# Kernel tuning notes

Hardware: AMD Instinct MI355X
Metric: run time of the kernel (lower is better)

## Reference

```python
import jax, jax.numpy as jnp
import numpy as np

N = 30000          # mesh vertices
B = 5 * 16         # p_bins * t_bins geodesic patch bins
NEURONS = [16, 64, 64, 32]


def setup_inputs() -> dict:
    key = jax.random.key(0)
    ks = jax.random.split(key, 7)
    x = jax.random.normal(ks[0], (N, NEURONS[0]), dtype=jnp.float32)
    conn = jax.random.randint(ks[1], (N, B), 0, N)  # per-vertex per-bin source index
    s1 = 1.0 / np.sqrt(NEURONS[0])
    W1 = jax.random.uniform(ks[2], (NEURONS[0], NEURONS[1]), minval=-s1, maxval=s1, dtype=jnp.float32)
    s2 = 1.0 / np.sqrt(B * NEURONS[1])
    Wg1 = jax.random.uniform(ks[3], (B, NEURONS[1], NEURONS[2]), minval=-s2, maxval=s2, dtype=jnp.float32)
    b1 = jax.random.uniform(ks[4], (NEURONS[2],), minval=-s2, maxval=s2, dtype=jnp.float32)
    s3 = 1.0 / np.sqrt(B * NEURONS[2])
    Wg2 = jax.random.uniform(ks[5], (B, NEURONS[2], NEURONS[3]), minval=-s3, maxval=s3, dtype=jnp.float32)
    b2 = jax.random.uniform(ks[6], (NEURONS[3],), minval=-s3, maxval=s3, dtype=jnp.float32)
    return {"x": x, "W1": W1, "Wg1": Wg1, "b1": b1, "Wg2": Wg2, "b2": b2, "conn": conn}


def _geodesic(h, conn, Wg, b):
    # gather geodesic patch: [N, B, C_in], then per-bin contraction
    patches = h[conn]                               # irregular gather
    return jnp.einsum("nbi,bio->no", patches, Wg) + b


def reference(x, W1, Wg1, b1, Wg2, b2, conn):
    h = jax.nn.relu(x @ W1)                         # linear_1 (no bias, l_bias=False)
    h = jax.nn.relu(_geodesic(h, conn, Wg1, b1))    # GC_1 + relu
    res = _geodesic(h, conn, Wg2, b2)               # GC_2
    norm = jnp.linalg.norm(res, axis=-1, keepdims=True)
    return res / norm
```

## Files before the change

### kernel.cpp

```cpp
#include <hip/hip_runtime.h>
#include <stdint.h>
#include <stddef.h>


typedef __attribute__((ext_vector_type(8))) short bf16x8;
typedef __attribute__((ext_vector_type(4))) float f32x4;

#define BINS 80

static __device__ __forceinline__ unsigned short f2bf(float f) {
  union { float f; unsigned int u; } c; c.f = f;
  unsigned int u = c.u;
  return (unsigned short)((u + 0x7FFFu + ((u >> 16) & 1u)) >> 16);
}

__global__ __launch_bounds__(256) void k_lin1(const float* __restrict__ x,
                                              const float* __restrict__ W1,
                                              unsigned short* __restrict__ h1b, int n) {
  __shared__ float w1s[16 * 64];
  int tid = threadIdx.x;
  for (int i = tid; i < 16 * 64; i += 256) w1s[i] = W1[i];
  __syncthreads();
  int v = blockIdx.x * 256 + tid;
  if (v >= n) return;
  const float4* xp = (const float4*)(x + (size_t)v * 16);
  float4 x0 = xp[0], x1 = xp[1], x2 = xp[2], x3 = xp[3];
  float xr[16] = {x0.x, x0.y, x0.z, x0.w, x1.x, x1.y, x1.z, x1.w,
                  x2.x, x2.y, x2.z, x2.w, x3.x, x3.y, x3.z, x3.w};
  float acc[64];
#pragma unroll
  for (int o = 0; o < 64; ++o) acc[o] = 0.f;
#pragma unroll
  for (int i = 0; i < 16; ++i) {
    float xi = xr[i];
#pragma unroll
    for (int o = 0; o < 64; ++o) acc[o] = fmaf(xi, w1s[i * 64 + o], acc[o]);
  }
  unsigned short* hr = h1b + (size_t)v * 64;
#pragma unroll
  for (int o8 = 0; o8 < 8; ++o8) {
    bf16x8 pack;
#pragma unroll
    for (int j = 0; j < 8; ++j) pack[j] = (short)f2bf(fmaxf(acc[o8 * 8 + j], 0.f));
    *(bf16x8*)(hr + o8 * 8) = pack;
  }
}

__global__ __launch_bounds__(256) void k_wimg(const float* __restrict__ Wg,
                                              unsigned char* __restrict__ img,
                                              int O, int total) {
  int t = blockIdx.x * 256 + threadIdx.x;
  if (t >= total) return;
  int c = t & 7;
  int o = (t >> 3) % O;
  int b = t / (O * 8);
  int boff = (o * 128 + c * 16) ^ ((o & 7) << 4);
  bf16x8 pack;
#pragma unroll
  for (int j = 0; j < 8; ++j)
    pack[j] = (short)f2bf(Wg[(size_t)(b * 64 + c * 8 + j) * O + o]);
  *(bf16x8*)(img + (size_t)b * (O * 128) + boff) = pack;
}

template <int OT, bool DO_NORM>
__global__ __launch_bounds__(256) void k_geo(const unsigned short* __restrict__ hin,
                                             const unsigned char* __restrict__ wimg,
                                             const float* __restrict__ bias,
                                             const int* __restrict__ conn,
                                             void* __restrict__ outp, int n) {
  constexpr int TILEB = OT * 16 * 128;
  __shared__ int conn_s[64 * 81];
  __shared__ alignas(16) unsigned char wg_s[2][TILEB];

  const int tid = threadIdx.x;
  const int lane = tid & 63;
  const int wave = tid >> 6;
  const int ln15 = lane & 15;
  const int lq = lane >> 4;
  const int v0 = blockIdx.x * 64;

  for (int idx = tid; idx < 64 * BINS; idx += 256) {
    int v = idx / BINS;
    int c = idx - v * BINS;
    int vv = v0 + v;
    if (vv > n - 1) vv = n - 1;
    conn_s[v * 81 + c] = conn[(size_t)vv * BINS + c];
  }

  auto stage = [&](int bin, int buf) {
    const unsigned char* src = wimg + (size_t)bin * TILEB + wave * (TILEB / 4) + lane * 16;
    unsigned char* dst = &wg_s[buf][wave * (TILEB / 4)];
#pragma unroll
    for (int i = 0; i < TILEB / 4096; ++i) {
      __builtin_amdgcn_global_load_lds(
          (const __attribute__((address_space(1))) unsigned int*)(const void*)(src + i * 1024),
          (__attribute__((address_space(3))) unsigned int*)(void*)(dst + i * 1024),
          16, 0, 0);
    }
  };

  int boffs[OT][2];
#pragma unroll
  for (int ot = 0; ot < OT; ++ot)
#pragma unroll
    for (int s = 0; s < 2; ++s) {
      int o = ot * 16 + ln15;
      boffs[ot][s] = (o * 128 + s * 64 + lq * 16) ^ ((o & 7) << 4);
    }

  f32x4 acc[OT];
#pragma unroll
  for (int ot = 0; ot < OT; ++ot) acc[ot] = (f32x4){0.f, 0.f, 0.f, 0.f};

  stage(0, 0);
  __syncthreads();

  const int crow = (wave * 16 + ln15) * 81;
  const int koff = lq * 8;

  for (int b = 0; b < BINS; ++b) {
    int cur = b & 1;
    if (b + 1 < BINS) stage(b + 1, cur ^ 1);

    int cidx = conn_s[crow + b];
    const unsigned short* arow = hin + (size_t)cidx * 64 + koff;
    bf16x8 a0 = *(const bf16x8*)(arow);
    bf16x8 a1 = *(const bf16x8*)(arow + 32);

    const unsigned char* wb = wg_s[cur];
#pragma unroll
    for (int ot = 0; ot < OT; ++ot) {
      bf16x8 b0 = *(const bf16x8*)(wb + boffs[ot][0]);
      bf16x8 b1 = *(const bf16x8*)(wb + boffs[ot][1]);
      acc[ot] = __builtin_amdgcn_mfma_f32_16x16x32_bf16(a0, b0, acc[ot], 0, 0, 0);
      acc[ot] = __builtin_amdgcn_mfma_f32_16x16x32_bf16(a1, b1, acc[ot], 0, 0, 0);
    }
    __syncthreads();
  }

  if constexpr (!DO_NORM) {
    unsigned short* hout = (unsigned short*)outp;
#pragma unroll
    for (int ot = 0; ot < OT; ++ot) {
      float bo = bias[ot * 16 + ln15];
#pragma unroll
      for (int r = 0; r < 4; ++r) {
        int v = v0 + wave * 16 + lq * 4 + r;
        if (v < n) {
          float val = fmaxf(acc[ot][r] + bo, 0.f);
          hout[(size_t)v * 64 + ot * 16 + ln15] = f2bf(val);
        }
      }
    }
  } else {
    float* outf = (float*)outp;
    float bo0 = bias[ln15];
    float bo1 = bias[16 + ln15];
#pragma unroll
    for (int r = 0; r < 4; ++r) {
      float a = acc[0][r] + bo0;
      float c2 = acc[1][r] + bo1;
      float ss = a * a + c2 * c2;
      ss += __shfl_xor(ss, 1);
      ss += __shfl_xor(ss, 2);
      ss += __shfl_xor(ss, 4);
      ss += __shfl_xor(ss, 8);
      float inv = 1.0f / sqrtf(ss);
      int v = v0 + wave * 16 + lq * 4 + r;
      if (v < n) {
        outf[(size_t)v * 32 + ln15] = a * inv;
        outf[(size_t)v * 32 + 16 + ln15] = c2 * inv;
      }
    }
  }
}

extern "C" void kernel_launch(void* const* d_in, const int* in_sizes, int n_in,
                              void* d_out, int out_size, void* d_ws, size_t ws_size,
                              hipStream_t stream) {
  const float* x   = (const float*)d_in[0];
  const float* W1  = (const float*)d_in[1];
  const float* Wg1 = (const float*)d_in[2];
  const float* b1  = (const float*)d_in[3];
  const float* Wg2 = (const float*)d_in[4];
  const float* b2  = (const float*)d_in[5];
  const int*  conn = (const int*)d_in[6];
  int n = in_sizes[0] / 16;

  unsigned char* ws = (unsigned char*)d_ws;
  size_t hb = (size_t)n * 64 * 2;
  unsigned short* h1b = (unsigned short*)(ws);
  unsigned short* h2b = (unsigned short*)(ws + hb);
  unsigned char*  w1i = ws + 2 * hb;
  unsigned char*  w2i = ws + 2 * hb + 80 * 8192;

  k_wimg<<<(80 * 64 * 8 + 255) / 256, 256, 0, stream>>>(Wg1, w1i, 64, 80 * 64 * 8);
  k_wimg<<<(80 * 32 * 8 + 255) / 256, 256, 0, stream>>>(Wg2, w2i, 32, 80 * 32 * 8);
  k_lin1<<<(n + 255) / 256, 256, 0, stream>>>(x, W1, h1b, n);

  int gb = (n + 63) / 64;
  k_geo<4, false><<<gb, 256, 0, stream>>>(h1b, w1i, b1, conn, (void*)h2b, n);
  k_geo<2, true><<<gb, 256, 0, stream>>>(h2b, w2i, b2, conn, d_out, n);
}
```

Measured before the change: 137.0 us.

## Split geodesic conv over bins into 4 chunks with reduction kernels and gather prefetch

Each geodesic conv now splits its 80 bins into 4 chunks along a second grid dimension, which gives 4x more blocks (469 to about 1876). Each block writes fp32 partial sums to workspace. Separate finalize kernels then add the partials, apply the bias and then either relu with bf16 packing or the L2 normalisation. The gathered rows for the next bin are also prefetched into registers one iteration ahead. The aim is better occupancy and latency hiding on the many CUs, at the cost of extra partial-sum traffic (about 30 MB for the first layer) and two more launches.

```diff
diff --git a/kernel.cpp b/kernel.cpp
--- a/kernel.cpp
+++ b/kernel.cpp
@@ -7,6 +7,8 @@
 typedef __attribute__((ext_vector_type(4))) float f32x4;
 
 #define BINS 80
+#define SPLITK 4
+#define BPC 20
 
 static __device__ __forceinline__ unsigned short f2bf(float f) {
   union { float f; unsigned int u; } c; c.f = f;
@@ -62,14 +64,13 @@
   *(bf16x8*)(img + (size_t)b * (O * 128) + boff) = pack;
 }
 
-template <int OT, bool DO_NORM>
-__global__ __launch_bounds__(256) void k_geo(const unsigned short* __restrict__ hin,
-                                             const unsigned char* __restrict__ wimg,
-                                             const float* __restrict__ bias,
-                                             const int* __restrict__ conn,
-                                             void* __restrict__ outp, int n) {
+template <int OT>
+__global__ __launch_bounds__(256) void k_geo_sk(const unsigned short* __restrict__ hin,
+                                                const unsigned char* __restrict__ wimg,
+                                                const int* __restrict__ conn,
+                                                float* __restrict__ part, int n) {
   constexpr int TILEB = OT * 16 * 128;
-  __shared__ int conn_s[64 * 81];
+  __shared__ int conn_s[64 * (BPC + 1)];
   __shared__ alignas(16) unsigned char wg_s[2][TILEB];
 
   const int tid = threadIdx.x;
@@ -78,13 +79,15 @@
   const int ln15 = lane & 15;
   const int lq = lane >> 4;
   const int v0 = blockIdx.x * 64;
-
-  for (int idx = tid; idx < 64 * BINS; idx += 256) {
-    int v = idx / BINS;
-    int c = idx - v * BINS;
+  const int chunk = blockIdx.y;
+  const int bin0 = chunk * BPC;
+
+  for (int idx = tid; idx < 64 * BPC; idx += 256) {
+    int v = idx / BPC;
+    int c = idx - v * BPC;
     int vv = v0 + v;
     if (vv > n - 1) vv = n - 1;
-    conn_s[v * 81 + c] = conn[(size_t)vv * BINS + c];
+    conn_s[v * (BPC + 1) + c] = conn[(size_t)vv * BINS + bin0 + c];
   }
 
   auto stage = [&](int bin, int buf) {
@@ -112,20 +115,30 @@
 #pragma unroll
   for (int ot = 0; ot < OT; ++ot) acc[ot] = (f32x4){0.f, 0.f, 0.f, 0.f};
 
-  stage(0, 0);
+  stage(bin0, 0);
   __syncthreads();
 
-  const int crow = (wave * 16 + ln15) * 81;
+  const int crow = (wave * 16 + ln15) * (BPC + 1);
   const int koff = lq * 8;
 
-  for (int b = 0; b < BINS; ++b) {
-    int cur = b & 1;
-    if (b + 1 < BINS) stage(b + 1, cur ^ 1);
-
-    int cidx = conn_s[crow + b];
+  bf16x8 a0, a1;
+  {
+    int cidx = conn_s[crow];
     const unsigned short* arow = hin + (size_t)cidx * 64 + koff;
-    bf16x8 a0 = *(const bf16x8*)(arow);
-    bf16x8 a1 = *(const bf16x8*)(arow + 32);
+    a0 = *(const bf16x8*)(arow);
+    a1 = *(const bf16x8*)(arow + 32);
+  }
+
+  for (int cb = 0; cb < BPC; ++cb) {
+    int cur = cb & 1;
+    bf16x8 na0 = a0, na1 = a1;
+    if (cb + 1 < BPC) {
+      stage(bin0 + cb + 1, cur ^ 1);
+      int nc = conn_s[crow + cb + 1];
+      const unsigned short* arow = hin + (size_t)nc * 64 + koff;
+      na0 = *(const bf16x8*)(arow);
+      na1 = *(const bf16x8*)(arow + 32);
+    }
 
     const unsigned char* wb = wg_s[cur];
 #pragma unroll
@@ -136,43 +149,70 @@
       acc[ot] = __builtin_amdgcn_mfma_f32_16x16x32_bf16(a1, b1, acc[ot], 0, 0, 0);
     }
     __syncthreads();
-  }
-
-  if constexpr (!DO_NORM) {
-    unsigned short* hout = (unsigned short*)outp;
-#pragma unroll
-    for (int ot = 0; ot < OT; ++ot) {
-      float bo = bias[ot * 16 + ln15];
-#pragma unroll
-      for (int r = 0; r < 4; ++r) {
-        int v = v0 + wave * 16 + lq * 4 + r;
-        if (v < n) {
-          float val = fmaxf(acc[ot][r] + bo, 0.f);
-          hout[(size_t)v * 64 + ot * 16 + ln15] = f2bf(val);
-        }
-      }
-    }
-  } else {
-    float* outf = (float*)outp;
-    float bo0 = bias[ln15];
-    float bo1 = bias[16 + ln15];
+    a0 = na0; a1 = na1;
+  }
+
+  constexpr int O = OT * 16;
+  float* pbase = part + (size_t)chunk * n * O;
+#pragma unroll
+  for (int ot = 0; ot < OT; ++ot) {
 #pragma unroll
     for (int r = 0; r < 4; ++r) {
-      float a = acc[0][r] + bo0;
-      float c2 = acc[1][r] + bo1;
-      float ss = a * a + c2 * c2;
-      ss += __shfl_xor(ss, 1);
-      ss += __shfl_xor(ss, 2);
-      ss += __shfl_xor(ss, 4);
-      ss += __shfl_xor(ss, 8);
-      float inv = 1.0f / sqrtf(ss);
       int v = v0 + wave * 16 + lq * 4 + r;
-      if (v < n) {
-        outf[(size_t)v * 32 + ln15] = a * inv;
-        outf[(size_t)v * 32 + 16 + ln15] = c2 * inv;
-      }
-    }
-  }
+      if (v < n) pbase[(size_t)v * O + ot * 16 + ln15] = acc[ot][r];
+    }
+  }
+}
+
+__global__ __launch_bounds__(256) void k_fin1(const float* __restrict__ part,
+                                              const float* __restrict__ bias,
+                                              unsigned short* __restrict__ out, int n) {
+  int t = blockIdx.x * 256 + threadIdx.x;
+  int total = n * 16;
+  if (t >= total) return;
+  int base = t * 4;
+  int o = base & 63;
+  size_t stride = (size_t)n * 64;
+  const float* p = part + base;
+  float4 s = *(const float4*)(p);
+#pragma unroll
+  for (int c = 1; c < SPLITK; ++c) {
+    float4 q = *(const float4*)(p + c * stride);
+    s.x += q.x; s.y += q.y; s.z += q.z; s.w += q.w;
+  }
+  float4 b4 = *(const float4*)(bias + o);
+  ushort4 pack;
+  pack.x = f2bf(fmaxf(s.x + b4.x, 0.f));
+  pack.y = f2bf(fmaxf(s.y + b4.y, 0.f));
+  pack.z = f2bf(fmaxf(s.z + b4.z, 0.f));
+  pack.w = f2bf(fmaxf(s.w + b4.w, 0.f));
+  *(ushort4*)(out + base) = pack;
+}
+
+__global__ __launch_bounds__(256) void k_fin2(const float* __restrict__ part,
+                                              const float* __restrict__ bias,
+                                              float* __restrict__ out, int n) {
+  int v = blockIdx.x * 16 + (threadIdx.x >> 4);
+  int o = threadIdx.x & 15;
+  if (v >= n) return;
+  size_t stride = (size_t)n * 32;
+  const float* p = part + (size_t)v * 32 + o;
+  float a = 0.f, b = 0.f;
+#pragma unroll
+  for (int c = 0; c < SPLITK; ++c) {
+    a += p[c * stride];
+    b += p[c * stride + 16];
+  }
+  a += bias[o];
+  b += bias[o + 16];
+  float ss = a * a + b * b;
+  ss += __shfl_xor(ss, 1);
+  ss += __shfl_xor(ss, 2);
+  ss += __shfl_xor(ss, 4);
+  ss += __shfl_xor(ss, 8);
+  float inv = 1.0f / sqrtf(ss);
+  out[(size_t)v * 32 + o] = a * inv;
+  out[(size_t)v * 32 + 16 + o] = b * inv;
 }
 
 extern "C" void kernel_launch(void* const* d_in, const int* in_sizes, int n_in,
@@ -188,17 +228,20 @@
   int n = in_sizes[0] / 16;
 
   unsigned char* ws = (unsigned char*)d_ws;
-  size_t hb = (size_t)n * 64 * 2;
+  size_t hb = ((size_t)n * 64 * 2 + 255) & ~(size_t)255;
   unsigned short* h1b = (unsigned short*)(ws);
   unsigned short* h2b = (unsigned short*)(ws + hb);
   unsigned char*  w1i = ws + 2 * hb;
   unsigned char*  w2i = ws + 2 * hb + 80 * 8192;
+  float* part = (float*)(ws + 2 * hb + 80 * 8192 + 80 * 4096);
 
   k_wimg<<<(80 * 64 * 8 + 255) / 256, 256, 0, stream>>>(Wg1, w1i, 64, 80 * 64 * 8);
   k_wimg<<<(80 * 32 * 8 + 255) / 256, 256, 0, stream>>>(Wg2, w2i, 32, 80 * 32 * 8);
   k_lin1<<<(n + 255) / 256, 256, 0, stream>>>(x, W1, h1b, n);
 
   int gb = (n + 63) / 64;
-  k_geo<4, false><<<gb, 256, 0, stream>>>(h1b, w1i, b1, conn, (void*)h2b, n);
-  k_geo<2, true><<<gb, 256, 0, stream>>>(h2b, w2i, b2, conn, d_out, n);
-}
+  k_geo_sk<4><<<dim3(gb, SPLITK), 256, 0, stream>>>(h1b, w1i, conn, part, n);
+  k_fin1<<<(n * 16 + 255) / 256, 256, 0, stream>>>(part, b1, h2b, n);
+  k_geo_sk<2><<<dim3(gb, SPLITK), 256, 0, stream>>>(h2b, w2i, conn, part, n);
+  k_fin2<<<(n + 15) / 16, 256, 0, stream>>>(part, b2, (float*)d_out, n);
+}
```

After: 140.4 us. 1.02x slower.
